# Kernel optimization log

Hardware: AMD Instinct MI355X
Metric: run time of the kernel (lower is better)

Reference implementation:

```python
import jax, jax.numpy as jnp
import numpy as np

BETA = 0.25
TEMP = 0.5  # softmax temperature divisor used in Codebook.forward


def setup_inputs() -> dict:
    key = jax.random.key(0)
    k1, k2 = jax.random.split(key)
    B, C, H, W = 16, 512, 28, 28
    num_pq, K = 4, 2048
    d = C // num_pq  # 128
    z = jax.random.normal(k1, (B, C, H, W), dtype=jnp.float32)
    # nn.Embedding init: uniform(-1/K, 1/K), one codebook per product quantizer
    codebooks = jax.random.uniform(k2, (num_pq, K, d), dtype=jnp.float32,
                                   minval=-1.0 / K, maxval=1.0 / K)
    return {"z": z, "codebooks": codebooks}


def reference(z, codebooks):
    B, C, H, W = z.shape
    P, K, d = codebooks.shape  # P product quantizers, K codes, d = C // P
    N = B * H * W

    # torch.chunk(z, P, dim=1) then permute(0,2,3,1).view(-1, d) per chunk
    # -> (P, N, d)
    zc = z.reshape(B, P, d, H, W)
    zf = jnp.transpose(zc, (1, 0, 3, 4, 2)).reshape(P, N, d)

    # normalize == 'none': z_norm = z_flat, codebook_norm = codebook
    # pairwise squared distances: ||z||^2 + ||c||^2 - 2 z c^T  -> (P, N, K)
    dist = (jnp.sum(zf * zf, axis=-1, keepdims=True)
            + jnp.sum(codebooks * codebooks, axis=-1)[:, None, :]
            - 2.0 * jnp.einsum('pnd,pkd->pnk', zf, codebooks))

    idx = jnp.argmin(dist, axis=-1)                      # (P, N)
    prob = jax.nn.softmax(-dist / TEMP, axis=-1)         # (P, N, K)

    # use_weighted_sum == False: z_q = embedding lookup
    zq = codebooks[jnp.arange(P)[:, None], idx]          # (P, N, d)

    # losses: mean over P of per-quantizer MSE == global MSE (equal sizes)
    codebook_loss = jnp.mean((zq - jax.lax.stop_gradient(zf)) ** 2)
    commitment_loss = jnp.mean((zf - jax.lax.stop_gradient(zq)) ** 2)
    q_loss = codebook_loss + BETA * commitment_loss

    # straight-through estimator
    zq_st = zf + jax.lax.stop_gradient(zq - zf)

    # back to (B, C, H, W): (P,N,d)->(P,B,H,W,d)->(B,P,d,H,W)->(B,C,H,W)
    zq_out = jnp.transpose(zq_st.reshape(P, B, H, W, d),
                           (1, 0, 4, 2, 3)).reshape(B, C, H, W)

    # distance_prob concat along last dim: (N, P*K)
    distance_prob = jnp.transpose(prob, (1, 0, 2)).reshape(N, P * K)

    return zq_out, q_loss, distance_prob
```

## Files before the change

kernel.cpp:

```cpp
#include <hip/hip_runtime.h>

#define P_    4
#define K_    2048
#define D_    128
#define B_    16
#define HW_   784
#define N_    (B_ * HW_)
#define C_    512

#define OUT0_SZ   (B_ * C_ * HW_)
#define QLOSS_OFF OUT0_SZ
#define OUT2_OFF  (OUT0_SZ + 1)

typedef short  short8 __attribute__((ext_vector_type(8)));
typedef float  f32x4  __attribute__((ext_vector_type(4)));

__device__ __forceinline__ short f2bf(float x) {
    union { float f; unsigned u; } a; a.f = x;
    unsigned r = a.u + 0x7FFF + ((a.u >> 16) & 1);
    return (short)(r >> 16);
}

__global__ __launch_bounds__(256) void vq_prep(const float* __restrict__ cb,
                                               short* __restrict__ cbb,
                                               float* __restrict__ cnorm) {
    int wave = threadIdx.x >> 6;
    int lane = threadIdx.x & 63;
    int row  = blockIdx.x * 4 + wave;
    const float* src = cb + (size_t)row * D_;
    float2 v = *(const float2*)(src + lane * 2);
    cbb[(size_t)row * D_ + lane * 2 + 0] = f2bf(v.x);
    cbb[(size_t)row * D_ + lane * 2 + 1] = f2bf(v.y);
    float s = v.x * v.x + v.y * v.y;
    #pragma unroll
    for (int m = 1; m < 64; m <<= 1) s += __shfl_xor(s, m, 64);
    if (lane == 0) cnorm[row] = s;
}

__global__ __launch_bounds__(512, 4) void vq_main(const float* __restrict__ z,
                                                  const short* __restrict__ cbb,
                                                  const float* __restrict__ cnorm,
                                                  const float* __restrict__ cb,
                                                  float* __restrict__ out0,
                                                  float* __restrict__ qloss,
                                                  float* __restrict__ out2) {
    __shared__ short As[16][136];
    __shared__ float wsum[8][16];
    __shared__ float wmax[8][16];
    __shared__ int   wmidx[8][16];
    __shared__ int   ridx[16];
    __shared__ float lsum[8];
    __shared__ float ps[4][2048];

    const int bx  = blockIdx.x;
    const int p   = bx / (N_ / 16);
    const int nt  = bx % (N_ / 16);
    const int b   = nt / 49;
    const int hw0 = (nt % 49) * 16;
    const int n0  = nt * 16;

    const int kz  = threadIdx.x >> 2;
    const int q4  = threadIdx.x & 3;
    float4 zv;
    {
        const float* src = z + ((size_t)b * C_ + p * D_ + kz) * HW_ + hw0 + q4 * 4;
        zv = *(const float4*)src;
        int r0 = q4 * 4;
        As[r0 + 0][kz] = f2bf(zv.x);  As[r0 + 1][kz] = f2bf(zv.y);
        As[r0 + 2][kz] = f2bf(zv.z);  As[r0 + 3][kz] = f2bf(zv.w);
    }
    __syncthreads();

    const int wave = threadIdx.x >> 6;
    const int lane = threadIdx.x & 63;
    const int llo  = lane & 15;
    const int lhi  = lane >> 4;

    short8 af[4];
    #pragma unroll
    for (int s = 0; s < 4; s++)
        af[s] = *(const short8*)&As[llo][s * 32 + lhi * 8];

    const short* bptr = cbb + ((size_t)(p * K_ + wave * 256 + llo) * D_ + lhi * 8);

    f32x4 acc[16];
    #pragma unroll
    for (int ct = 0; ct < 16; ct++) {
        const short* bp = bptr + (size_t)ct * 16 * D_;
        short8 b0 = *(const short8*)(bp +  0);
        short8 b1 = *(const short8*)(bp + 32);
        short8 b2 = *(const short8*)(bp + 64);
        short8 b3 = *(const short8*)(bp + 96);
        f32x4 a = {0.f, 0.f, 0.f, 0.f};
        a = __builtin_amdgcn_mfma_f32_16x16x32_bf16(af[0], b0, a, 0, 0, 0);
        a = __builtin_amdgcn_mfma_f32_16x16x32_bf16(af[1], b1, a, 0, 0, 0);
        a = __builtin_amdgcn_mfma_f32_16x16x32_bf16(af[2], b2, a, 0, 0, 0);
        a = __builtin_amdgcn_mfma_f32_16x16x32_bf16(af[3], b3, a, 0, 0, 0);
        acc[ct] = a;
    }

    float rs[4] = {0.f, 0.f, 0.f, 0.f};
    float mx[4] = {-1e30f, -1e30f, -1e30f, -1e30f};
    int   mi[4] = {0, 0, 0, 0};
    const float* cn = cnorm + p * K_ + wave * 256 + llo;
    #pragma unroll
    for (int ct = 0; ct < 16; ct++) {
        float c = cn[ct * 16];
        #pragma unroll
        for (int r = 0; r < 4; r++) {
            float s = 4.0f * acc[ct][r] - 2.0f * c;
            float e = __expf(s);
            acc[ct][r] = e;
            rs[r] += e;
            if (e > mx[r]) { mx[r] = e; mi[r] = wave * 256 + ct * 16 + llo; }
        }
    }
    #pragma unroll
    for (int m = 1; m < 16; m <<= 1) {
        #pragma unroll
        for (int r = 0; r < 4; r++) {
            rs[r] += __shfl_xor(rs[r], m, 64);
            float om = __shfl_xor(mx[r], m, 64);
            int   oi = __shfl_xor(mi[r], m, 64);
            if (om > mx[r] || (om == mx[r] && oi < mi[r])) { mx[r] = om; mi[r] = oi; }
        }
    }
    if (llo == 0) {
        #pragma unroll
        for (int r = 0; r < 4; r++) {
            int row = lhi * 4 + r;
            wsum[wave][row]  = rs[r];
            wmax[wave][row]  = mx[r];
            wmidx[wave][row] = mi[r];
        }
    }
    __syncthreads();

    float inv[4];
    #pragma unroll
    for (int r = 0; r < 4; r++) {
        int row = lhi * 4 + r;
        float s = 0.f;
        #pragma unroll
        for (int w2 = 0; w2 < 8; w2++) s += wsum[w2][row];
        inv[r] = 1.0f / s;
    }
    if (threadIdx.x < 16) {
        int row = threadIdx.x;
        float m0 = wmax[0][row]; int i0 = wmidx[0][row];
        #pragma unroll
        for (int w2 = 1; w2 < 8; w2++) {
            float mm = wmax[w2][row]; int ii = wmidx[w2][row];
            if (mm > m0 || (mm == m0 && ii < i0)) { m0 = mm; i0 = ii; }
        }
        ridx[row] = i0;
    }
    __syncthreads();

    {
        const float* cbp = cb + ((size_t)p * K_) * D_ + kz;
        float4 q;
        q.x = cbp[(size_t)ridx[q4 * 4 + 0] * D_];
        q.y = cbp[(size_t)ridx[q4 * 4 + 1] * D_];
        q.z = cbp[(size_t)ridx[q4 * 4 + 2] * D_];
        q.w = cbp[(size_t)ridx[q4 * 4 + 3] * D_];
        float* dst = out0 + ((size_t)b * C_ + p * D_ + kz) * HW_ + hw0 + q4 * 4;
        *(float4*)dst = q;
        float dx = q.x - zv.x, dy = q.y - zv.y;
        float dz = q.z - zv.z, dw = q.w - zv.w;
        float loss = dx * dx + dy * dy + dz * dz + dw * dw;
        #pragma unroll
        for (int m = 1; m < 64; m <<= 1) loss += __shfl_xor(loss, m, 64);
        if (lane == 0) lsum[wave] = loss;
    }
    __syncthreads();
    if (threadIdx.x == 0) {
        float tot = 0.f;
        #pragma unroll
        for (int w2 = 0; w2 < 8; w2++) tot += lsum[w2];
        atomicAdd(qloss, tot * (1.25f / (float)(P_ * (size_t)N_ * D_)));
    }

    #pragma unroll
    for (int g = 0; g < 4; g++) {
        __syncthreads();
        if (lhi == g) {
            #pragma unroll
            for (int ct = 0; ct < 16; ct++) {
                #pragma unroll
                for (int r = 0; r < 4; r++)
                    ps[r][wave * 256 + ct * 16 + llo] = acc[ct][r] * inv[r];
            }
        }
        __syncthreads();
        {
            int row = threadIdx.x >> 7;
            int c4  = (threadIdx.x & 127) * 4;
            float* orow = out2 + (size_t)(n0 + g * 4 + row) * (P_ * K_) + p * K_;
            #pragma unroll
            for (int k = 0; k < 4; k++) {
                f32x4 v = *(const f32x4*)&ps[row][c4 + k * 512];
                *(f32x4*)(orow + c4 + k * 512) = v;
            }
        }
    }
}

extern "C" void kernel_launch(void* const* d_in, const int* in_sizes, int n_in,
                              void* d_out, int out_size, void* d_ws, size_t ws_size,
                              hipStream_t stream) {
    const float* z  = (const float*)d_in[0];
    const float* cb = (const float*)d_in[1];
    float* out = (float*)d_out;

    float* ws_cnorm = (float*)((char*)d_ws + (256 << 10));
    short* ws_cbb   = (short*)((char*)d_ws + (512 << 10));

    hipMemsetAsync(out + QLOSS_OFF, 0, sizeof(float), stream);
    vq_prep<<<(P_ * K_) / 4, 256, 0, stream>>>(cb, ws_cbb, ws_cnorm);
    vq_main<<<P_ * (N_ / 16), 512, 0, stream>>>(z, ws_cbb, ws_cnorm, cb,
                                                out, out + QLOSS_OFF,
                                                out + OUT2_OFF);
}
```

Measured before the change: 632.6 us.

## Swap MFMA operands so each lane holds 4 contiguous codes, store probs directly

Swaps the A/B operands of the bf16 MFMA so that each lane's accumulator holds four consecutive codebook entries for a single z row, not one code across four rows. Softmax statistics then need only cross-lane reductions over lhi. The probability output can be written straight from registers as float4 stores, dropping the 32KB shared staging buffer and its eight barriers. Each 16-byte store now covers a 64-byte row segment per lane group and rows are scattered, so write coalescing is weaker than the previous full-row staged stores.

New measurement: 742.8 us. 17.4% more time.

```diff
diff --git a/kernel.cpp b/kernel.cpp
--- a/kernel.cpp
+++ b/kernel.cpp
@@ -50,7 +50,6 @@
     __shared__ int   wmidx[8][16];
     __shared__ int   ridx[16];
     __shared__ float lsum[8];
-    __shared__ float ps[4][2048];
 
     const int bx  = blockIdx.x;
     const int p   = bx / (N_ / 16);
@@ -76,10 +75,10 @@
     const int llo  = lane & 15;
     const int lhi  = lane >> 4;
 
-    short8 af[4];
+    short8 zf[4];
     #pragma unroll
     for (int s = 0; s < 4; s++)
-        af[s] = *(const short8*)&As[llo][s * 32 + lhi * 8];
+        zf[s] = *(const short8*)&As[llo][s * 32 + lhi * 8];
 
     const short* bptr = cbb + ((size_t)(p * K_ + wave * 256 + llo) * D_ + lhi * 8);
 
@@ -92,59 +91,48 @@
         short8 b2 = *(const short8*)(bp + 64);
         short8 b3 = *(const short8*)(bp + 96);
         f32x4 a = {0.f, 0.f, 0.f, 0.f};
-        a = __builtin_amdgcn_mfma_f32_16x16x32_bf16(af[0], b0, a, 0, 0, 0);
-        a = __builtin_amdgcn_mfma_f32_16x16x32_bf16(af[1], b1, a, 0, 0, 0);
-        a = __builtin_amdgcn_mfma_f32_16x16x32_bf16(af[2], b2, a, 0, 0, 0);
-        a = __builtin_amdgcn_mfma_f32_16x16x32_bf16(af[3], b3, a, 0, 0, 0);
+        a = __builtin_amdgcn_mfma_f32_16x16x32_bf16(b0, zf[0], a, 0, 0, 0);
+        a = __builtin_amdgcn_mfma_f32_16x16x32_bf16(b1, zf[1], a, 0, 0, 0);
+        a = __builtin_amdgcn_mfma_f32_16x16x32_bf16(b2, zf[2], a, 0, 0, 0);
+        a = __builtin_amdgcn_mfma_f32_16x16x32_bf16(b3, zf[3], a, 0, 0, 0);
         acc[ct] = a;
     }
 
-    float rs[4] = {0.f, 0.f, 0.f, 0.f};
-    float mx[4] = {-1e30f, -1e30f, -1e30f, -1e30f};
-    int   mi[4] = {0, 0, 0, 0};
-    const float* cn = cnorm + p * K_ + wave * 256 + llo;
+    float rs = 0.f;
+    float mx = -1e30f;
+    int   mi = 0;
+    const float* cnp = cnorm + p * K_ + wave * 256 + lhi * 4;
     #pragma unroll
     for (int ct = 0; ct < 16; ct++) {
-        float c = cn[ct * 16];
+        f32x4 c4 = *(const f32x4*)(cnp + ct * 16);
         #pragma unroll
         for (int r = 0; r < 4; r++) {
-            float s = 4.0f * acc[ct][r] - 2.0f * c;
+            float s = 4.0f * acc[ct][r] - 2.0f * c4[r];
             float e = __expf(s);
             acc[ct][r] = e;
-            rs[r] += e;
-            if (e > mx[r]) { mx[r] = e; mi[r] = wave * 256 + ct * 16 + llo; }
+            rs += e;
+            if (e > mx) { mx = e; mi = wave * 256 + ct * 16 + lhi * 4 + r; }
         }
     }
     #pragma unroll
-    for (int m = 1; m < 16; m <<= 1) {
-        #pragma unroll
-        for (int r = 0; r < 4; r++) {
-            rs[r] += __shfl_xor(rs[r], m, 64);
-            float om = __shfl_xor(mx[r], m, 64);
-            int   oi = __shfl_xor(mi[r], m, 64);
-            if (om > mx[r] || (om == mx[r] && oi < mi[r])) { mx[r] = om; mi[r] = oi; }
-        }
+    for (int m = 16; m < 64; m <<= 1) {
+        rs += __shfl_xor(rs, m, 64);
+        float om = __shfl_xor(mx, m, 64);
+        int   oi = __shfl_xor(mi, m, 64);
+        if (om > mx || (om == mx && oi < mi)) { mx = om; mi = oi; }
     }
-    if (llo == 0) {
-        #pragma unroll
-        for (int r = 0; r < 4; r++) {
-            int row = lhi * 4 + r;
-            wsum[wave][row]  = rs[r];
-            wmax[wave][row]  = mx[r];
-            wmidx[wave][row] = mi[r];
-        }
+    if (lhi == 0) {
+        wsum[wave][llo]  = rs;
+        wmax[wave][llo]  = mx;
+        wmidx[wave][llo] = mi;
     }
     __syncthreads();
 
-    float inv[4];
+    float ssum = 0.f;
     #pragma unroll
-    for (int r = 0; r < 4; r++) {
-        int row = lhi * 4 + r;
-        float s = 0.f;
-        #pragma unroll
-        for (int w2 = 0; w2 < 8; w2++) s += wsum[w2][row];
-        inv[r] = 1.0f / s;
-    }
+    for (int w2 = 0; w2 < 8; w2++) ssum += wsum[w2][llo];
+    const float inv = 1.0f / ssum;
+
     if (threadIdx.x < 16) {
         int row = threadIdx.x;
         float m0 = wmax[0][row]; int i0 = wmidx[0][row];
@@ -181,28 +169,11 @@
         atomicAdd(qloss, tot * (1.25f / (float)(P_ * (size_t)N_ * D_)));
     }
 
+    float* obase = out2 + (size_t)(n0 + llo) * (P_ * K_) + p * K_ + wave * 256 + lhi * 4;
     #pragma unroll
-    for (int g = 0; g < 4; g++) {
-        __syncthreads();
-        if (lhi == g) {
-            #pragma unroll
-            for (int ct = 0; ct < 16; ct++) {
-                #pragma unroll
-                for (int r = 0; r < 4; r++)
-                    ps[r][wave * 256 + ct * 16 + llo] = acc[ct][r] * inv[r];
-            }
-        }
-        __syncthreads();
-        {
-            int row = threadIdx.x >> 7;
-            int c4  = (threadIdx.x & 127) * 4;
-            float* orow = out2 + (size_t)(n0 + g * 4 + row) * (P_ * K_) + p * K_;
-            #pragma unroll
-            for (int k = 0; k < 4; k++) {
-                f32x4 v = *(const f32x4*)&ps[row][c4 + k * 512];
-                *(f32x4*)(orow + c4 + k * 512) = v;
-            }
-        }
+    for (int ct = 0; ct < 16; ct++) {
+        f32x4 v = acc[ct] * inv;
+        *(f32x4*)(obase + ct * 16) = v;
     }
 }
 
```
